# Kernel tuning notes

Hardware: AMD Instinct MI355X
Metric: run time of the kernel (lower is better)

Reference implementation:

```python
import jax, jax.numpy as jnp
import numpy as np

TINY = 1e-6  # TINY_NUMBER in the original repo

def setup_inputs() -> dict:
    key = jax.random.key(0)
    ks = jax.random.split(key, 12)
    R, S, N, D = 2048, 64, 10, 32
    H = D // 8
    def w(kk, i, o):
        return (jax.random.normal(kk, (i, o), jnp.float32) / np.sqrt(i)).astype(jnp.float32)
    return {
        "q": jax.random.normal(ks[0], (R, S, D), jnp.float32),
        "k": jax.random.normal(ks[1], (R, S, N, D), jnp.float32),
        "pos": jax.random.normal(ks[2], (R, S, N, 4), jnp.float32),
        "mask": jax.random.randint(ks[3], (R, S, N, 1), 0, 2, jnp.int32),
        "Wq": w(ks[4], D, D), "Wk": w(ks[5], D, D), "Wv": w(ks[6], D, D),
        "pW1": w(ks[7], 4, H), "pb1": jnp.zeros((H,), jnp.float32),
        "pW2": w(ks[8], H, D), "pb2": jnp.zeros((D,), jnp.float32),
        "aW1": w(ks[9], D, H), "ab1": jnp.zeros((H,), jnp.float32),
        "aW2": w(ks[10], H, D), "ab2": jnp.zeros((D,), jnp.float32),
        "oW": w(ks[11], D, D), "ob": jnp.zeros((D,), jnp.float32),
    }

def reference(q, k, pos, mask, Wq, Wk, Wv, pW1, pb1, pW2, pb2, aW1, ab1, aW2, ab2, oW, ob):
    # q:[R,S,D] k:[R,S,N,D] pos:[R,S,N,4] mask:[R,S,N,1]
    R, S, N, D = k.shape
    qp = q @ Wq                       # [R,S,D]
    kp = k @ Wk                       # [R,S,N,D]
    vp = k @ Wv                       # [R,S,N,D]

    valid = (mask != 0)[..., 0]       # [R,S,N]
    cnt = valid.sum(-1)               # [R,S] valid count per group
    all_inv = cnt == 0                # rows with no valid src: torch code resets mask to all-valid
    valid_eff = valid | all_inv[..., None]
    cnt_eff = jnp.where(all_inv, N, cnt)

    wm = valid_eff[..., None].astype(kp.dtype)          # [R,S,N,1]
    cntf = cnt_eff[..., None].astype(kp.dtype)          # [R,S,1]
    mean = (kp * wm).sum(2) / cntf                      # masked mean over valid src
    var = (wm * (kp - mean[:, :, None, :]) ** 2).sum(2) / jnp.maximum(cntf - 1.0, 1.0)  # unbiased (ddof=1), like torch.std
    mean_abs = (wm * jnp.abs(kp)).sum(2) / cntf
    single = (cnt_eff == 1)[..., None]                  # valid_cnt==1 -> zeros in torch code
    std = jnp.sqrt(jnp.where(single, 1.0, var))
    k_std = jnp.where(single, 0.0, std)                 # [R,S,D]
    normalized_k_std = jnp.where(single, 0.0, std / (mean_abs + TINY))

    pemb = jax.nn.relu(pos @ pW1 + pb1) @ pW2 + pb2     # [R,S,N,D]
    scores = kp - qp[:, :, None, :] + pemb
    scores = jax.nn.relu(scores @ aW1 + ab1) @ aW2 + ab2
    scores = jnp.where(valid_eff[..., None], scores, -jnp.inf)
    attn = jax.nn.softmax(scores, axis=2)               # softmax over n_src; no fully -inf rows by construction

    x = ((vp + pemb) * attn).sum(2) @ oW + ob           # [R,S,D]; dropout is identity at eval
    return x, attn, k_std, normalized_k_std
```

## Files before the change

### kernel.cpp

```cpp
#include <hip/hip_runtime.h>
#include <math.h>

#define NG 8
#define NSRC 10
#define DIM 32

__launch_bounds__(256, 2)
__global__ void attn2d_kernel(
    const float* __restrict__ q, const float* __restrict__ k,
    const float* __restrict__ pos, const int* __restrict__ mask,
    const float* __restrict__ Wq, const float* __restrict__ Wk,
    const float* __restrict__ Wv,
    const float* __restrict__ pW1, const float* __restrict__ pb1,
    const float* __restrict__ pW2, const float* __restrict__ pb2,
    const float* __restrict__ aW1, const float* __restrict__ ab1,
    const float* __restrict__ aW2, const float* __restrict__ ab2,
    const float* __restrict__ oW, const float* __restrict__ ob,
    float* __restrict__ out_x, float* __restrict__ out_attn,
    float* __restrict__ out_std, float* __restrict__ out_nks)
{
    __shared__ float4 Wq4[256];
    __shared__ float4 Wk4[256];
    __shared__ float4 Wv4[256];
    __shared__ float4 Wo4[256];
    __shared__ float4 kb4[NG * NSRC * 8];
    __shared__ float4 qb4[NG * 8];
    __shared__ float4 posb[NG * NSRC];
    __shared__ float4 ub4[NG * NSRC];
    __shared__ float4 pw1c[4];
    __shared__ float4 pw2t[32];
    __shared__ float4 aw1col[32];
    __shared__ float4 aw2t[32];
    __shared__ int    mb[NG * NSRC];
    __shared__ float  pb1b[4];
    __shared__ float  ab1b[4];
    __shared__ float  pb2b[32];
    __shared__ float  ab2b[32];
    __shared__ float  obb[32];
    __shared__ float  yb[NG * DIM];

    const int tid = threadIdx.x;
    const int gb  = tid >> 5;
    const int d   = tid & 31;
    const long long G0 = (long long)blockIdx.x * NG + gb;

    {
        const int cc = gb, dd = d;
        Wq4[tid] = make_float4(Wq[(4*cc+0)*32+dd], Wq[(4*cc+1)*32+dd],
                               Wq[(4*cc+2)*32+dd], Wq[(4*cc+3)*32+dd]);
        Wk4[tid] = make_float4(Wk[(4*cc+0)*32+dd], Wk[(4*cc+1)*32+dd],
                               Wk[(4*cc+2)*32+dd], Wk[(4*cc+3)*32+dd]);
        Wv4[tid] = make_float4(Wv[(4*cc+0)*32+dd], Wv[(4*cc+1)*32+dd],
                               Wv[(4*cc+2)*32+dd], Wv[(4*cc+3)*32+dd]);
        Wo4[tid] = make_float4(oW[(4*cc+0)*32+dd], oW[(4*cc+1)*32+dd],
                               oW[(4*cc+2)*32+dd], oW[(4*cc+3)*32+dd]);

        const float4* kg4 = (const float4*)k;
        const long long kbase = (long long)blockIdx.x * (NG * NSRC * 8);
        #pragma unroll
        for (int r = 0; r < 3; ++r) {
            int i = tid + r * 256;
            if (i < NG * NSRC * 8) kb4[i] = kg4[kbase + i];
        }
        if (tid < NG * 8)
            qb4[tid] = ((const float4*)q)[(long long)blockIdx.x * NG * 8 + tid];
        if (tid < NG * NSRC) {
            posb[tid] = ((const float4*)pos)[(long long)blockIdx.x * NG * NSRC + tid];
            mb[tid]   = mask[(long long)blockIdx.x * NG * NSRC + tid];
        }
        if (tid < 4) {
            pw1c[tid] = make_float4(pW1[0*4+tid], pW1[1*4+tid], pW1[2*4+tid], pW1[3*4+tid]);
            pb1b[tid] = pb1[tid];
            ab1b[tid] = ab1[tid];
        }
        if (tid < 32) {
            pw2t[tid] = make_float4(pW2[0*32+tid], pW2[1*32+tid], pW2[2*32+tid], pW2[3*32+tid]);
            pb2b[tid] = pb2[tid];
            aw2t[tid] = make_float4(aW2[0*32+tid], aW2[1*32+tid], aW2[2*32+tid], aW2[3*32+tid]);
            ab2b[tid] = ab2[tid];
            obb[tid]  = ob[tid];
            int h = tid & 3, c = tid >> 2;
            aw1col[tid] = make_float4(aW1[(4*c+0)*4+h], aW1[(4*c+1)*4+h],
                                      aW1[(4*c+2)*4+h], aW1[(4*c+3)*4+h]);
        }
    }
    __syncthreads();

    float pe[NSRC];
    {
        const float4 pw1r0 = pw1c[0], pw1r1 = pw1c[1], pw1r2 = pw1c[2], pw1r3 = pw1c[3];
        const float pb10 = pb1b[0], pb11 = pb1b[1], pb12 = pb1b[2], pb13 = pb1b[3];
        const float4 pw2d = pw2t[d]; const float pb2d = pb2b[d];
        #pragma unroll
        for (int n = 0; n < NSRC; ++n) {
            float4 p4 = posb[gb*NSRC + n];
            float t0 = fmaxf(pb10 + p4.x*pw1r0.x + p4.y*pw1r0.y + p4.z*pw1r0.z + p4.w*pw1r0.w, 0.f);
            float t1 = fmaxf(pb11 + p4.x*pw1r1.x + p4.y*pw1r1.y + p4.z*pw1r1.z + p4.w*pw1r1.w, 0.f);
            float t2 = fmaxf(pb12 + p4.x*pw1r2.x + p4.y*pw1r2.y + p4.z*pw1r2.z + p4.w*pw1r2.w, 0.f);
            float t3 = fmaxf(pb13 + p4.x*pw1r3.x + p4.y*pw1r3.y + p4.z*pw1r3.z + p4.w*pw1r3.w, 0.f);
            pe[n] = pb2d + t0*pw2d.x + t1*pw2d.y + t2*pw2d.z + t3*pw2d.w;
        }
    }

    unsigned vbits = 0; int cnt = 0;
    #pragma unroll
    for (int n = 0; n < NSRC; ++n) {
        int m = mb[gb*NSRC + n];
        vbits |= (unsigned)(m != 0) << n;
        cnt += (m != 0);
    }
    if (cnt == 0) { vbits = (1u << NSRC) - 1u; cnt = NSRC; }

    float qp = 0.f;
    float kp[NSRC], vp[NSRC];
    #pragma unroll
    for (int n = 0; n < NSRC; ++n) { kp[n] = 0.f; vp[n] = 0.f; }

    #pragma unroll 2
    for (int c = 0; c < 8; ++c) {
        float4 wq = Wq4[c*32 + d];
        float4 wk = Wk4[c*32 + d];
        float4 wv = Wv4[c*32 + d];
        float4 q4 = qb4[gb*8 + c];
        qp += q4.x*wq.x + q4.y*wq.y + q4.z*wq.z + q4.w*wq.w;
        #pragma unroll
        for (int n = 0; n < NSRC; ++n) {
            float4 kk = kb4[(gb*NSRC+n)*8 + c];
            kp[n] += kk.x*wk.x + kk.y*wk.y + kk.z*wk.z + kk.w*wk.w;
            vp[n] += kk.x*wv.x + kk.y*wv.y + kk.z*wv.z + kk.w*wv.w;
        }
    }

    {
        const float cntf = (float)cnt;
        const float rc = 1.f / cntf;
        float mean = 0.f, mabs = 0.f;
        #pragma unroll
        for (int n = 0; n < NSRC; ++n) {
            float w = (float)((vbits >> n) & 1u);
            mean += w * kp[n]; mabs += w * fabsf(kp[n]);
        }
        mean *= rc; mabs *= rc;
        float var = 0.f;
        #pragma unroll
        for (int n = 0; n < NSRC; ++n) {
            float w = (float)((vbits >> n) & 1u);
            float dd2 = kp[n] - mean; var += w * dd2 * dd2;
        }
        var *= 1.f / fmaxf(cntf - 1.f, 1.f);
        const float stdv = (cnt == 1) ? 0.f : sqrtf(var);
        const float nksv = (cnt == 1) ? 0.f : stdv / (mabs + 1e-6f);
        out_std[G0*DIM + d] = stdv;
        out_nks[G0*DIM + d] = nksv;
    }

    #pragma unroll
    for (int n = 0; n < NSRC; ++n) vp[n] += pe[n];

    float* scb = (float*)kb4;
    #pragma unroll
    for (int n = 0; n < NSRC; ++n) {
        int idx = (((d >> 2) ^ (n & 7)) << 2) | (d & 3);
        scb[(gb*NSRC + n)*DIM + idx] = kp[n] - qp + pe[n];
    }

    {
        const float4* scb4 = (const float4*)kb4;
        float* ub = (float*)ub4;
        int n = d >> 2, h = d & 3;
        float u = ab1b[h];
        #pragma unroll
        for (int c = 0; c < 8; ++c) {
            float4 s4 = scb4[(gb*NSRC + n)*8 + (c ^ (n & 7))];
            float4 a4 = aw1col[c*4 + h];
            u += s4.x*a4.x + s4.y*a4.y + s4.z*a4.z + s4.w*a4.w;
        }
        ub[gb*NSRC*4 + n*4 + h] = fmaxf(u, 0.f);
        if (d < 8) {
            int n2 = 8 + (d >> 2);
            float u2 = ab1b[h];
            #pragma unroll
            for (int c = 0; c < 8; ++c) {
                float4 s4 = scb4[(gb*NSRC + n2)*8 + (c ^ (n2 & 7))];
                float4 a4 = aw1col[c*4 + h];
                u2 += s4.x*a4.x + s4.y*a4.y + s4.z*a4.z + s4.w*a4.w;
            }
            ub[gb*NSRC*4 + n2*4 + h] = fmaxf(u2, 0.f);
        }
    }

    float at[NSRC];
    {
        const float4 aw2d = aw2t[d]; const float ab2d = ab2b[d];
        #pragma unroll
        for (int n = 0; n < NSRC; ++n) {
            float4 r4 = ub4[gb*NSRC + n];
            float s = ab2d + r4.x*aw2d.x + r4.y*aw2d.y + r4.z*aw2d.z + r4.w*aw2d.w;
            at[n] = ((vbits >> n) & 1u) ? s : -INFINITY;
        }
    }
    float mx = at[0];
    #pragma unroll
    for (int n = 1; n < NSRC; ++n) mx = fmaxf(mx, at[n]);
    float ssum = 0.f;
    #pragma unroll
    for (int n = 0; n < NSRC; ++n) { float e = __expf(at[n]-mx); at[n] = e; ssum += e; }
    const float rs = 1.f / ssum;

    float y = 0.f;
    {
        const long long abase = G0*(NSRC*DIM) + d;
        #pragma unroll
        for (int n = 0; n < NSRC; ++n) {
            float a = at[n] * rs;
            y += vp[n] * a;
            out_attn[abase + n*DIM] = a;
        }
    }
    yb[gb*DIM + d] = y;
    {
        const float4* yb4 = (const float4*)yb;
        float x = obb[d];
        #pragma unroll
        for (int c = 0; c < 8; ++c) {
            float4 wo = Wo4[c*32 + d];
            float4 y4 = yb4[gb*8 + c];
            x += y4.x*wo.x + y4.y*wo.y + y4.z*wo.z + y4.w*wo.w;
        }
        out_x[G0*DIM + d] = x;
    }
}

extern "C" void kernel_launch(void* const* d_in, const int* in_sizes, int n_in,
                              void* d_out, int out_size, void* d_ws, size_t ws_size,
                              hipStream_t stream) {
    const float* q    = (const float*)d_in[0];
    const float* k    = (const float*)d_in[1];
    const float* pos  = (const float*)d_in[2];
    const int*   mask = (const int*)  d_in[3];
    const float* Wq   = (const float*)d_in[4];
    const float* Wk   = (const float*)d_in[5];
    const float* Wv   = (const float*)d_in[6];
    const float* pW1  = (const float*)d_in[7];
    const float* pb1  = (const float*)d_in[8];
    const float* pW2  = (const float*)d_in[9];
    const float* pb2  = (const float*)d_in[10];
    const float* aW1  = (const float*)d_in[11];
    const float* ab1  = (const float*)d_in[12];
    const float* aW2  = (const float*)d_in[13];
    const float* ab2  = (const float*)d_in[14];
    const float* oW   = (const float*)d_in[15];
    const float* ob   = (const float*)d_in[16];

    const int G = in_sizes[0] / DIM;
    const int blocks = G / NG;

    float* out_x    = (float*)d_out;
    float* out_attn = out_x + (long long)G * DIM;
    float* out_std  = out_attn + (long long)G * NSRC * DIM;
    float* out_nks  = out_std + (long long)G * DIM;

    attn2d_kernel<<<blocks, 256, 0, stream>>>(
        q, k, pos, mask, Wq, Wk, Wv, pW1, pb1, pW2, pb2,
        aW1, ab1, aW2, ab2, oW, ob,
        out_x, out_attn, out_std, out_nks);
}
```

Measured before the change: 574.6 us.

## Process multiple tiles per block with packed k/v FMA and hoisted pos MLP

Each block now loops over four group tiles, so the shared-memory weight staging (Wq, Wk/Wv, oW and the small MLP weights) is paid once per four tiles instead of once per tile. Wk and Wv are interleaved into one shared array so the k and v projections run as packed two-wide FMAs. The first layer of the position MLP is now computed once per source position during the load phase rather than redundantly in every lane, and the output staging buffer reuses ub4. In exchange, there are four times fewer blocks and no prefetch of the next tile, so global loads within a block are serialized with compute behind extra barriers.

```diff
diff --git a/kernel.cpp b/kernel.cpp
--- a/kernel.cpp
+++ b/kernel.cpp
@@ -4,6 +4,9 @@
 #define NG 8
 #define NSRC 10
 #define DIM 32
+#define TILES 4
+
+typedef float floatx2 __attribute__((ext_vector_type(2)));
 
 __launch_bounds__(256, 2)
 __global__ void attn2d_kernel(
@@ -20,59 +23,36 @@
     float* __restrict__ out_std, float* __restrict__ out_nks)
 {
     __shared__ float4 Wq4[256];
-    __shared__ float4 Wk4[256];
-    __shared__ float4 Wv4[256];
+    __shared__ float4 Wkv4[512];
     __shared__ float4 Wo4[256];
     __shared__ float4 kb4[NG * NSRC * 8];
     __shared__ float4 qb4[NG * 8];
     __shared__ float4 posb[NG * NSRC];
     __shared__ float4 ub4[NG * NSRC];
-    __shared__ float4 pw1c[4];
     __shared__ float4 pw2t[32];
     __shared__ float4 aw1col[32];
     __shared__ float4 aw2t[32];
     __shared__ int    mb[NG * NSRC];
-    __shared__ float  pb1b[4];
     __shared__ float  ab1b[4];
     __shared__ float  pb2b[32];
     __shared__ float  ab2b[32];
     __shared__ float  obb[32];
-    __shared__ float  yb[NG * DIM];
 
     const int tid = threadIdx.x;
     const int gb  = tid >> 5;
     const int d   = tid & 31;
-    const long long G0 = (long long)blockIdx.x * NG + gb;
 
     {
         const int cc = gb, dd = d;
         Wq4[tid] = make_float4(Wq[(4*cc+0)*32+dd], Wq[(4*cc+1)*32+dd],
                                Wq[(4*cc+2)*32+dd], Wq[(4*cc+3)*32+dd]);
-        Wk4[tid] = make_float4(Wk[(4*cc+0)*32+dd], Wk[(4*cc+1)*32+dd],
-                               Wk[(4*cc+2)*32+dd], Wk[(4*cc+3)*32+dd]);
-        Wv4[tid] = make_float4(Wv[(4*cc+0)*32+dd], Wv[(4*cc+1)*32+dd],
-                               Wv[(4*cc+2)*32+dd], Wv[(4*cc+3)*32+dd]);
+        Wkv4[(2*cc+0)*32+dd] = make_float4(Wk[(4*cc+0)*32+dd], Wv[(4*cc+0)*32+dd],
+                                           Wk[(4*cc+1)*32+dd], Wv[(4*cc+1)*32+dd]);
+        Wkv4[(2*cc+1)*32+dd] = make_float4(Wk[(4*cc+2)*32+dd], Wv[(4*cc+2)*32+dd],
+                                           Wk[(4*cc+3)*32+dd], Wv[(4*cc+3)*32+dd]);
         Wo4[tid] = make_float4(oW[(4*cc+0)*32+dd], oW[(4*cc+1)*32+dd],
                                oW[(4*cc+2)*32+dd], oW[(4*cc+3)*32+dd]);
-
-        const float4* kg4 = (const float4*)k;
-        const long long kbase = (long long)blockIdx.x * (NG * NSRC * 8);
-        #pragma unroll
-        for (int r = 0; r < 3; ++r) {
-            int i = tid + r * 256;
-            if (i < NG * NSRC * 8) kb4[i] = kg4[kbase + i];
-        }
-        if (tid < NG * 8)
-            qb4[tid] = ((const float4*)q)[(long long)blockIdx.x * NG * 8 + tid];
-        if (tid < NG * NSRC) {
-            posb[tid] = ((const float4*)pos)[(long long)blockIdx.x * NG * NSRC + tid];
-            mb[tid]   = mask[(long long)blockIdx.x * NG * NSRC + tid];
-        }
-        if (tid < 4) {
-            pw1c[tid] = make_float4(pW1[0*4+tid], pW1[1*4+tid], pW1[2*4+tid], pW1[3*4+tid]);
-            pb1b[tid] = pb1[tid];
-            ab1b[tid] = ab1[tid];
-        }
+        if (tid < 4) ab1b[tid] = ab1[tid];
         if (tid < 32) {
             pw2t[tid] = make_float4(pW2[0*32+tid], pW2[1*32+tid], pW2[2*32+tid], pW2[3*32+tid]);
             pb2b[tid] = pb2[tid];
@@ -84,150 +64,176 @@
                                       aW1[(4*c+2)*4+h], aW1[(4*c+3)*4+h]);
         }
     }
-    __syncthreads();
-
-    float pe[NSRC];
-    {
-        const float4 pw1r0 = pw1c[0], pw1r1 = pw1c[1], pw1r2 = pw1c[2], pw1r3 = pw1c[3];
-        const float pb10 = pb1b[0], pb11 = pb1b[1], pb12 = pb1b[2], pb13 = pb1b[3];
-        const float4 pw2d = pw2t[d]; const float pb2d = pb2b[d];
+
+    #pragma unroll 1
+    for (int t = 0; t < TILES; ++t) {
+        const long long tb = (long long)blockIdx.x * TILES + t;
+        const long long G0 = tb * NG + gb;
+
+        if (t > 0) __syncthreads();
+
+        {
+            const float4* kg4 = (const float4*)k;
+            const long long kbase = tb * (NG * NSRC * 8);
+            #pragma unroll
+            for (int r = 0; r < 3; ++r) {
+                int i = tid + r * 256;
+                if (i < NG * NSRC * 8) kb4[i] = kg4[kbase + i];
+            }
+            if (tid < NG * 8)
+                qb4[tid] = ((const float4*)q)[tb * NG * 8 + tid];
+            if (tid < NG * NSRC) {
+                float4 p4 = ((const float4*)pos)[tb * NG * NSRC + tid];
+                float t0 = fmaxf(pb1[0] + p4.x*pW1[0*4+0] + p4.y*pW1[1*4+0] + p4.z*pW1[2*4+0] + p4.w*pW1[3*4+0], 0.f);
+                float t1 = fmaxf(pb1[1] + p4.x*pW1[0*4+1] + p4.y*pW1[1*4+1] + p4.z*pW1[2*4+1] + p4.w*pW1[3*4+1], 0.f);
+                float t2 = fmaxf(pb1[2] + p4.x*pW1[0*4+2] + p4.y*pW1[1*4+2] + p4.z*pW1[2*4+2] + p4.w*pW1[3*4+2], 0.f);
+                float t3 = fmaxf(pb1[3] + p4.x*pW1[0*4+3] + p4.y*pW1[1*4+3] + p4.z*pW1[2*4+3] + p4.w*pW1[3*4+3], 0.f);
+                posb[tid] = make_float4(t0, t1, t2, t3);
+                mb[tid]   = mask[tb * NG * NSRC + tid];
+            }
+        }
+        __syncthreads();
+
+        float pe[NSRC];
+        {
+            const float4 pw2d = pw2t[d]; const float pb2d = pb2b[d];
+            #pragma unroll
+            for (int n = 0; n < NSRC; ++n) {
+                float4 h4 = posb[gb*NSRC + n];
+                pe[n] = pb2d + h4.x*pw2d.x + h4.y*pw2d.y + h4.z*pw2d.z + h4.w*pw2d.w;
+            }
+        }
+
+        unsigned vbits = 0; int cnt = 0;
         #pragma unroll
         for (int n = 0; n < NSRC; ++n) {
-            float4 p4 = posb[gb*NSRC + n];
-            float t0 = fmaxf(pb10 + p4.x*pw1r0.x + p4.y*pw1r0.y + p4.z*pw1r0.z + p4.w*pw1r0.w, 0.f);
-            float t1 = fmaxf(pb11 + p4.x*pw1r1.x + p4.y*pw1r1.y + p4.z*pw1r1.z + p4.w*pw1r1.w, 0.f);
-            float t2 = fmaxf(pb12 + p4.x*pw1r2.x + p4.y*pw1r2.y + p4.z*pw1r2.z + p4.w*pw1r2.w, 0.f);
-            float t3 = fmaxf(pb13 + p4.x*pw1r3.x + p4.y*pw1r3.y + p4.z*pw1r3.z + p4.w*pw1r3.w, 0.f);
-            pe[n] = pb2d + t0*pw2d.x + t1*pw2d.y + t2*pw2d.z + t3*pw2d.w;
-        }
-    }
-
-    unsigned vbits = 0; int cnt = 0;
-    #pragma unroll
-    for (int n = 0; n < NSRC; ++n) {
-        int m = mb[gb*NSRC + n];
-        vbits |= (unsigned)(m != 0) << n;
-        cnt += (m != 0);
-    }
-    if (cnt == 0) { vbits = (1u << NSRC) - 1u; cnt = NSRC; }
-
-    float qp = 0.f;
-    float kp[NSRC], vp[NSRC];
-    #pragma unroll
-    for (int n = 0; n < NSRC; ++n) { kp[n] = 0.f; vp[n] = 0.f; }
-
-    #pragma unroll 2
-    for (int c = 0; c < 8; ++c) {
-        float4 wq = Wq4[c*32 + d];
-        float4 wk = Wk4[c*32 + d];
-        float4 wv = Wv4[c*32 + d];
-        float4 q4 = qb4[gb*8 + c];
-        qp += q4.x*wq.x + q4.y*wq.y + q4.z*wq.z + q4.w*wq.w;
+            int m = mb[gb*NSRC + n];
+            vbits |= (unsigned)(m != 0) << n;
+            cnt += (m != 0);
+        }
+        if (cnt == 0) { vbits = (1u << NSRC) - 1u; cnt = NSRC; }
+
+        float qp = 0.f;
+        floatx2 kpv[NSRC];
+        #pragma unroll
+        for (int n = 0; n < NSRC; ++n) kpv[n] = floatx2{0.f, 0.f};
+
+        #pragma unroll 2
+        for (int c = 0; c < 8; ++c) {
+            float4 wq = Wq4[c*32 + d];
+            float4 wa = Wkv4[(2*c+0)*32 + d];
+            float4 wb = Wkv4[(2*c+1)*32 + d];
+            float4 q4 = qb4[gb*8 + c];
+            qp += q4.x*wq.x + q4.y*wq.y + q4.z*wq.z + q4.w*wq.w;
+            #pragma unroll
+            for (int n = 0; n < NSRC; ++n) {
+                float4 kk = kb4[(gb*NSRC+n)*8 + c];
+                kpv[n] = __builtin_elementwise_fma(floatx2{kk.x, kk.x}, floatx2{wa.x, wa.y}, kpv[n]);
+                kpv[n] = __builtin_elementwise_fma(floatx2{kk.y, kk.y}, floatx2{wa.z, wa.w}, kpv[n]);
+                kpv[n] = __builtin_elementwise_fma(floatx2{kk.z, kk.z}, floatx2{wb.x, wb.y}, kpv[n]);
+                kpv[n] = __builtin_elementwise_fma(floatx2{kk.w, kk.w}, floatx2{wb.z, wb.w}, kpv[n]);
+            }
+        }
+
+        {
+            const float cntf = (float)cnt;
+            const float rc = 1.f / cntf;
+            float mean = 0.f, mabs = 0.f;
+            #pragma unroll
+            for (int n = 0; n < NSRC; ++n) {
+                float w = (float)((vbits >> n) & 1u);
+                mean += w * kpv[n].x; mabs += w * fabsf(kpv[n].x);
+            }
+            mean *= rc; mabs *= rc;
+            float var = 0.f;
+            #pragma unroll
+            for (int n = 0; n < NSRC; ++n) {
+                float w = (float)((vbits >> n) & 1u);
+                float dd2 = kpv[n].x - mean; var += w * dd2 * dd2;
+            }
+            var *= 1.f / fmaxf(cntf - 1.f, 1.f);
+            const float stdv = (cnt == 1) ? 0.f : sqrtf(var);
+            const float nksv = (cnt == 1) ? 0.f : stdv / (mabs + 1e-6f);
+            out_std[G0*DIM + d] = stdv;
+            out_nks[G0*DIM + d] = nksv;
+        }
+
+        #pragma unroll
+        for (int n = 0; n < NSRC; ++n) kpv[n].y += pe[n];
+
+        float* scb = (float*)kb4;
         #pragma unroll
         for (int n = 0; n < NSRC; ++n) {
-            float4 kk = kb4[(gb*NSRC+n)*8 + c];
-            kp[n] += kk.x*wk.x + kk.y*wk.y + kk.z*wk.z + kk.w*wk.w;
-            vp[n] += kk.x*wv.x + kk.y*wv.y + kk.z*wv.z + kk.w*wv.w;
-        }
-    }
-
-    {
-        const float cntf = (float)cnt;
-        const float rc = 1.f / cntf;
-        float mean = 0.f, mabs = 0.f;
-        #pragma unroll
-        for (int n = 0; n < NSRC; ++n) {
-            float w = (float)((vbits >> n) & 1u);
-            mean += w * kp[n]; mabs += w * fabsf(kp[n]);
-        }
-        mean *= rc; mabs *= rc;
-        float var = 0.f;
-        #pragma unroll
-        for (int n = 0; n < NSRC; ++n) {
-            float w = (float)((vbits >> n) & 1u);
-            float dd2 = kp[n] - mean; var += w * dd2 * dd2;
-        }
-        var *= 1.f / fmaxf(cntf - 1.f, 1.f);
-        const float stdv = (cnt == 1) ? 0.f : sqrtf(var);
-        const float nksv = (cnt == 1) ? 0.f : stdv / (mabs + 1e-6f);
-        out_std[G0*DIM + d] = stdv;
-        out_nks[G0*DIM + d] = nksv;
-    }
-
-    #pragma unroll
-    for (int n = 0; n < NSRC; ++n) vp[n] += pe[n];
-
-    float* scb = (float*)kb4;
-    #pragma unroll
-    for (int n = 0; n < NSRC; ++n) {
-        int idx = (((d >> 2) ^ (n & 7)) << 2) | (d & 3);
-        scb[(gb*NSRC + n)*DIM + idx] = kp[n] - qp + pe[n];
-    }
-
-    {
-        const float4* scb4 = (const float4*)kb4;
-        float* ub = (float*)ub4;
-        int n = d >> 2, h = d & 3;
-        float u = ab1b[h];
-        #pragma unroll
-        for (int c = 0; c < 8; ++c) {
-            float4 s4 = scb4[(gb*NSRC + n)*8 + (c ^ (n & 7))];
-            float4 a4 = aw1col[c*4 + h];
-            u += s4.x*a4.x + s4.y*a4.y + s4.z*a4.z + s4.w*a4.w;
-        }
-        ub[gb*NSRC*4 + n*4 + h] = fmaxf(u, 0.f);
-        if (d < 8) {
-            int n2 = 8 + (d >> 2);
-            float u2 = ab1b[h];
+            int idx = (((d >> 2) ^ (n & 7)) << 2) | (d & 3);
+            scb[(gb*NSRC + n)*DIM + idx] = kpv[n].x - qp + pe[n];
+        }
+
+        {
+            const float4* scb4 = (const float4*)kb4;
+            float* ub = (float*)ub4;
+            int n = d >> 2, h = d & 3;
+            float u = ab1b[h];
             #pragma unroll
             for (int c = 0; c < 8; ++c) {
-                float4 s4 = scb4[(gb*NSRC + n2)*8 + (c ^ (n2 & 7))];
+                float4 s4 = scb4[(gb*NSRC + n)*8 + (c ^ (n & 7))];
                 float4 a4 = aw1col[c*4 + h];
-                u2 += s4.x*a4.x + s4.y*a4.y + s4.z*a4.z + s4.w*a4.w;
-            }
-            ub[gb*NSRC*4 + n2*4 + h] = fmaxf(u2, 0.f);
-        }
-    }
-
-    float at[NSRC];
-    {
-        const float4 aw2d = aw2t[d]; const float ab2d = ab2b[d];
-        #pragma unroll
-        for (int n = 0; n < NSRC; ++n) {
-            float4 r4 = ub4[gb*NSRC + n];
-            float s = ab2d + r4.x*aw2d.x + r4.y*aw2d.y + r4.z*aw2d.z + r4.w*aw2d.w;
-            at[n] = ((vbits >> n) & 1u) ? s : -INFINITY;
-        }
-    }
-    float mx = at[0];
-    #pragma unroll
-    for (int n = 1; n < NSRC; ++n) mx = fmaxf(mx, at[n]);
-    float ssum = 0.f;
-    #pragma unroll
-    for (int n = 0; n < NSRC; ++n) { float e = __expf(at[n]-mx); at[n] = e; ssum += e; }
-    const float rs = 1.f / ssum;
-
-    float y = 0.f;
-    {
-        const long long abase = G0*(NSRC*DIM) + d;
-        #pragma unroll
-        for (int n = 0; n < NSRC; ++n) {
-            float a = at[n] * rs;
-            y += vp[n] * a;
-            out_attn[abase + n*DIM] = a;
-        }
-    }
-    yb[gb*DIM + d] = y;
-    {
-        const float4* yb4 = (const float4*)yb;
-        float x = obb[d];
-        #pragma unroll
-        for (int c = 0; c < 8; ++c) {
-            float4 wo = Wo4[c*32 + d];
-            float4 y4 = yb4[gb*8 + c];
-            x += y4.x*wo.x + y4.y*wo.y + y4.z*wo.z + y4.w*wo.w;
-        }
-        out_x[G0*DIM + d] = x;
+                u += s4.x*a4.x + s4.y*a4.y + s4.z*a4.z + s4.w*a4.w;
+            }
+            ub[gb*NSRC*4 + n*4 + h] = fmaxf(u, 0.f);
+            if (d < 8) {
+                int n2 = 8 + (d >> 2);
+                float u2 = ab1b[h];
+                #pragma unroll
+                for (int c = 0; c < 8; ++c) {
+                    float4 s4 = scb4[(gb*NSRC + n2)*8 + (c ^ (n2 & 7))];
+                    float4 a4 = aw1col[c*4 + h];
+                    u2 += s4.x*a4.x + s4.y*a4.y + s4.z*a4.z + s4.w*a4.w;
+                }
+                ub[gb*NSRC*4 + n2*4 + h] = fmaxf(u2, 0.f);
+            }
+        }
+
+        float at[NSRC];
+        {
+            const float4 aw2d = aw2t[d]; const float ab2d = ab2b[d];
+            #pragma unroll
+            for (int n = 0; n < NSRC; ++n) {
+                float4 r4 = ub4[gb*NSRC + n];
+                float s = ab2d + r4.x*aw2d.x + r4.y*aw2d.y + r4.z*aw2d.z + r4.w*aw2d.w;
+                at[n] = ((vbits >> n) & 1u) ? s : -INFINITY;
+            }
+        }
+        float mx = at[0];
+        #pragma unroll
+        for (int n = 1; n < NSRC; ++n) mx = fmaxf(mx, at[n]);
+        float ssum = 0.f;
+        #pragma unroll
+        for (int n = 0; n < NSRC; ++n) { float e = __expf(at[n]-mx); at[n] = e; ssum += e; }
+        const float rs = 1.f / ssum;
+
+        float y = 0.f;
+        {
+            const long long abase = G0*(NSRC*DIM) + d;
+            #pragma unroll
+            for (int n = 0; n < NSRC; ++n) {
+                float a = at[n] * rs;
+                y += kpv[n].y * a;
+                out_attn[abase + n*DIM] = a;
+            }
+        }
+        float* ybg = (float*)(ub4 + gb*NSRC);
+        ybg[d] = y;
+        {
+            const float4* ybg4 = (const float4*)ybg;
+            float x = obb[d];
+            #pragma unroll
+            for (int c = 0; c < 8; ++c) {
+                float4 wo = Wo4[c*32 + d];
+                float4 y4 = ybg4[c];
+                x += y4.x*wo.x + y4.y*wo.y + y4.z*wo.z + y4.w*wo.w;
+            }
+            out_x[G0*DIM + d] = x;
+        }
     }
 }
 
@@ -253,7 +259,7 @@
     const float* ob   = (const float*)d_in[16];
 
     const int G = in_sizes[0] / DIM;
-    const int blocks = G / NG;
+    const int blocks = G / (NG * TILES);
 
     float* out_x    = (float*)d_out;
     float* out_attn = out_x + (long long)G * DIM;
```

After: 524.8 us. -8.7%, faster.
